# Kernel tuning notes

Measured on AMD Instinct MI355X. Metric: run time of the kernel, lower is better.

The kernel has to match this reference:

```python
import jax, jax.numpy as jnp
import numpy as np

D = 4       # number of TT dimensions
N = 128     # mode size per dimension (Ns)
R = 16      # TT rank (RMAX)
B = 262144  # batch of query points


def setup_inputs() -> dict:
    key = jax.random.key(0)
    ks = jax.random.split(key, 5)
    # points in [-1, 1] (remap_needed=True assumes this domain)
    x = jax.random.uniform(ks[0], (B, D), dtype=jnp.float32) * 2.0 - 1.0
    core0 = jax.random.normal(ks[1], (1, N, R), dtype=jnp.float32)
    core1 = jax.random.normal(ks[2], (R, N, R), dtype=jnp.float32)
    core2 = jax.random.normal(ks[3], (R, N, R), dtype=jnp.float32)
    core3 = jax.random.normal(ks[4], (R, N, 1), dtype=jnp.float32)
    return {"x": x, "core0": core0, "core1": core1, "core2": core2, "core3": core3}


def _forward(x, cores):
    # remap: (x + 1) / 2 * (Ns[0] - 1)  (module uses Ns[0] for all dims)
    n0 = cores[0].shape[1]
    xr = (x + 1.0) * 0.5 * (n0 - 1)
    # per-dim clamp to [0, Ns[i]-1]
    ns = jnp.array([c.shape[1] for c in cores], dtype=x.dtype)  # [D]
    xc = jnp.clip(xr, 0.0, ns - 1.0)  # broadcast over D
    idx_low = jnp.floor(xc).astype(jnp.int32)   # [B, D]
    idx_high = jnp.ceil(xc).astype(jnp.int32)   # [B, D]
    wh = xc - idx_low.astype(x.dtype)           # [B, D] interpolation weights
    # gather + linear interpolation per core -> list of [r_prev, B, r_next]
    newcores = []
    for i, c in enumerate(cores):
        lo = jnp.take(c, idx_low[:, i], axis=1)   # [r_prev, B, r_next]
        hi = jnp.take(c, idx_high[:, i], axis=1)  # [r_prev, B, r_next]
        w = wh[:, i][None, :, None]               # [1, B, 1]
        newcores.append((1.0 - w) * lo + w * hi)
    # chained batched contraction, right to left (matches ttcontract)
    res = newcores[-1]
    for i in range(len(newcores) - 2, 0, -1):
        res = jnp.einsum('abc,cbk->abk', newcores[i], res)
    return jnp.einsum('abc,cbk->b', newcores[0], res)  # [B]


def reference(x, core0, core1, core2, core3):
    return _forward(x, [core0, core1, core2, core3])
```

## Files before the change

### kernel.cpp

```cpp
#include <hip/hip_runtime.h>
#include <hip/hip_bf16.h>

typedef unsigned int uint32;

#define NPT 128
#define RNK 16
#define MIDROW 264
#define MIDROW_U32 132
#define EDGEROW 20
#define SMEM_BYTES (2*NPT*MIDROW*2 + 2*NPT*EDGEROW*4)

__device__ __forceinline__ float bl(uint32 u){ return __uint_as_float(u << 16); }
__device__ __forceinline__ float bh(uint32 u){ return __uint_as_float(u & 0xffff0000u); }

__device__ __forceinline__ float dot16(const float* v, uint4 U0, uint4 U1) {
  float s0 = fmaf(v[1],  bh(U0.x), v[0]*bl(U0.x));
  s0 = fmaf(v[2],  bl(U0.y), s0); s0 = fmaf(v[3],  bh(U0.y), s0);
  float s1 = fmaf(v[5],  bh(U0.z), v[4]*bl(U0.z));
  s1 = fmaf(v[6],  bl(U0.w), s1); s1 = fmaf(v[7],  bh(U0.w), s1);
  float s2 = fmaf(v[9],  bh(U1.x), v[8]*bl(U1.x));
  s2 = fmaf(v[10], bl(U1.y), s2); s2 = fmaf(v[11], bh(U1.y), s2);
  float s3 = fmaf(v[13], bh(U1.z), v[12]*bl(U1.z));
  s3 = fmaf(v[14], bl(U1.w), s3); s3 = fmaf(v[15], bh(U1.w), s3);
  return (s0 + s1) + (s2 + s3);
}

__device__ __forceinline__ void tt_mid(const uint32* __restrict__ base, float xc, float v[16]) {
  int n0 = (int)xc;
  float w = xc - (float)n0;
  int n1 = min(n0 + 1, NPT - 1);
  const uint32* r0 = base + n0 * MIDROW_U32;
  const uint32* r1 = base + n1 * MIDROW_U32;
  float nv[16];
#pragma unroll
  for (int j = 0; j < 16; ++j) {
    const uint4* p0 = (const uint4*)(r0 + j * 8);
    const uint4* p1 = (const uint4*)(r1 + j * 8);
    uint4 A0 = p0[0], A1 = p0[1];
    uint4 B0 = p1[0], B1 = p1[1];
    float a = dot16(v, A0, A1);
    float b = dot16(v, B0, B1);
    nv[j] = fmaf(w, b - a, a);
  }
#pragma unroll
  for (int j = 0; j < 16; ++j) v[j] = nv[j];
}

__device__ __forceinline__ float remap_clamp(float x) {
  float xr = (x + 1.0f) * 0.5f * (float)(NPT - 1);
  return fminf(fmaxf(xr, 0.0f), (float)(NPT - 1));
}

__global__ __launch_bounds__(1024) void tt_kernel(
    const float* __restrict__ x,  const float* __restrict__ g0,
    const float* __restrict__ g1, const float* __restrict__ g2,
    const float* __restrict__ g3, float* __restrict__ out, int npts)
{
  extern __shared__ char smem[];
  unsigned short* c1 = (unsigned short*)smem;
  unsigned short* c2 = c1 + NPT * MIDROW;
  float* c0 = (float*)(c2 + NPT * MIDROW);
  float* c3 = c0 + NPT * EDGEROW;

  for (int t = threadIdx.x; t < RNK * NPT * RNK; t += blockDim.x) {
    int i = t >> 11;
    int n = (t >> 4) & (NPT - 1);
    int j = t & (RNK - 1);
    __hip_bfloat16 h1 = __float2bfloat16(g1[t]);
    __hip_bfloat16 h2 = __float2bfloat16(g2[t]);
    c1[n * MIDROW + j * 16 + i] = *(unsigned short*)&h1;
    c2[n * MIDROW + j * 16 + i] = *(unsigned short*)&h2;
  }
  for (int t = threadIdx.x; t < NPT * RNK; t += blockDim.x) {
    int n = t >> 4;
    int i = t & (RNK - 1);
    c0[n * EDGEROW + i] = g0[t];
    c3[n * EDGEROW + i] = g3[i * NPT + n];
  }
  __syncthreads();

  int p = blockIdx.x * blockDim.x + threadIdx.x;
  if (p >= npts) return;
  float4 xv = reinterpret_cast<const float4*>(x)[p];

  float v[16];
  {
    float xc = remap_clamp(xv.x);
    int n0 = (int)xc; float w = xc - (float)n0; int n1 = min(n0 + 1, NPT - 1);
    const float4* L = (const float4*)(c0 + n0 * EDGEROW);
    const float4* H = (const float4*)(c0 + n1 * EDGEROW);
#pragma unroll
    for (int k = 0; k < 4; ++k) {
      float4 l = L[k], h = H[k];
      v[4*k+0] = fmaf(w, h.x - l.x, l.x);
      v[4*k+1] = fmaf(w, h.y - l.y, l.y);
      v[4*k+2] = fmaf(w, h.z - l.z, l.z);
      v[4*k+3] = fmaf(w, h.w - l.w, l.w);
    }
  }
  tt_mid((const uint32*)c1, remap_clamp(xv.y), v);
  tt_mid((const uint32*)c2, remap_clamp(xv.z), v);
  float acc;
  {
    float xc = remap_clamp(xv.w);
    int n0 = (int)xc; float w = xc - (float)n0; int n1 = min(n0 + 1, NPT - 1);
    const float4* L = (const float4*)(c3 + n0 * EDGEROW);
    const float4* H = (const float4*)(c3 + n1 * EDGEROW);
    float a0 = 0.f, a1 = 0.f, a2 = 0.f, a3 = 0.f;
#pragma unroll
    for (int k = 0; k < 4; ++k) {
      float4 l = L[k], h = H[k];
      a0 = fmaf(v[4*k+0], fmaf(w, h.x - l.x, l.x), a0);
      a1 = fmaf(v[4*k+1], fmaf(w, h.y - l.y, l.y), a1);
      a2 = fmaf(v[4*k+2], fmaf(w, h.z - l.z, l.z), a2);
      a3 = fmaf(v[4*k+3], fmaf(w, h.w - l.w, l.w), a3);
    }
    acc = (a0 + a1) + (a2 + a3);
  }
  out[p] = acc;
}

extern "C" void kernel_launch(void* const* d_in, const int* in_sizes, int n_in,
                              void* d_out, int out_size, void* d_ws, size_t ws_size,
                              hipStream_t stream) {
  const float* x  = (const float*)d_in[0];
  const float* g0 = (const float*)d_in[1];
  const float* g1 = (const float*)d_in[2];
  const float* g2 = (const float*)d_in[3];
  const float* g3 = (const float*)d_in[4];
  float* out = (float*)d_out;

  int B = in_sizes[0] / 4;
  hipFuncSetAttribute(reinterpret_cast<const void*>(tt_kernel),
                      hipFuncAttributeMaxDynamicSharedMemorySize, SMEM_BYTES);
  int block = 1024;
  int grid = (B + block - 1) / block;
  tt_kernel<<<grid, block, SMEM_BYTES, stream>>>(x, g0, g1, g2, g3, out, B);
}
```

Measured before the change: 92.56 us.

## Split each point across 8 lanes with LDS vector exchange and bf16 dot2

Each TT point is now handled by 8 cooperating threads instead of one. Each lane computes 2 of the 16 rank outputs per middle core, and the intermediate vector is exchanged through a per-wave LDS scratch area as packed bf16. The middle cores are stored in a new interleaved layout and, when the builtin is available, use the hardware bf16 dot2 instruction. Each block loops over 8 rounds of 128 points, with a shuffle reduction for the final core. This cuts per-thread register and LDS traffic, but quantizes the intermediate vector to bf16 and adds exchange and synchronisation overhead.

```diff
diff --git a/kernel.cpp b/kernel.cpp
--- a/kernel.cpp
+++ b/kernel.cpp
@@ -2,48 +2,48 @@
 #include <hip/hip_bf16.h>
 
 typedef unsigned int uint32;
+typedef unsigned short u16;
 
 #define NPT 128
 #define RNK 16
-#define MIDROW 264
-#define MIDROW_U32 132
+#define ROW_U16 256
 #define EDGEROW 20
-#define SMEM_BYTES (2*NPT*MIDROW*2 + 2*NPT*EDGEROW*4)
+#define NWAVES 16
+#define SMEM_BYTES (2*NPT*ROW_U16*2 + 2*NPT*EDGEROW*4 + NWAVES*64*4)
+
+#if defined(__has_builtin)
+#if __has_builtin(__builtin_amdgcn_fdot2_f32_bf16)
+#define HAVE_BFDOT2 1
+#endif
+#endif
 
 __device__ __forceinline__ float bl(uint32 u){ return __uint_as_float(u << 16); }
 __device__ __forceinline__ float bh(uint32 u){ return __uint_as_float(u & 0xffff0000u); }
 
-__device__ __forceinline__ float dot16(const float* v, uint4 U0, uint4 U1) {
-  float s0 = fmaf(v[1],  bh(U0.x), v[0]*bl(U0.x));
-  s0 = fmaf(v[2],  bl(U0.y), s0); s0 = fmaf(v[3],  bh(U0.y), s0);
-  float s1 = fmaf(v[5],  bh(U0.z), v[4]*bl(U0.z));
-  s1 = fmaf(v[6],  bl(U0.w), s1); s1 = fmaf(v[7],  bh(U0.w), s1);
-  float s2 = fmaf(v[9],  bh(U1.x), v[8]*bl(U1.x));
-  s2 = fmaf(v[10], bl(U1.y), s2); s2 = fmaf(v[11], bh(U1.y), s2);
-  float s3 = fmaf(v[13], bh(U1.z), v[12]*bl(U1.z));
-  s3 = fmaf(v[14], bl(U1.w), s3); s3 = fmaf(v[15], bh(U1.w), s3);
-  return (s0 + s1) + (s2 + s3);
+#ifdef HAVE_BFDOT2
+typedef __bf16 v2bf __attribute__((ext_vector_type(2)));
+__device__ __forceinline__ v2bf bc(uint32 u){ return __builtin_bit_cast(v2bf, u); }
+__device__ __forceinline__ float dot8(const uint32* vp, uint4 U) {
+  float s = 0.f;
+  s = __builtin_amdgcn_fdot2_f32_bf16(bc(vp[0]), bc(U.x), s, false);
+  s = __builtin_amdgcn_fdot2_f32_bf16(bc(vp[1]), bc(U.y), s, false);
+  s = __builtin_amdgcn_fdot2_f32_bf16(bc(vp[2]), bc(U.z), s, false);
+  s = __builtin_amdgcn_fdot2_f32_bf16(bc(vp[3]), bc(U.w), s, false);
+  return s;
 }
+#else
+__device__ __forceinline__ float dot8(const uint32* vp, uint4 U) {
+  float s = fmaf(bh(vp[0]), bh(U.x), bl(vp[0]) * bl(U.x));
+  s = fmaf(bl(vp[1]), bl(U.y), s); s = fmaf(bh(vp[1]), bh(U.y), s);
+  s = fmaf(bl(vp[2]), bl(U.z), s); s = fmaf(bh(vp[2]), bh(U.z), s);
+  s = fmaf(bl(vp[3]), bl(U.w), s); s = fmaf(bh(vp[3]), bh(U.w), s);
+  return s;
+}
+#endif
 
-__device__ __forceinline__ void tt_mid(const uint32* __restrict__ base, float xc, float v[16]) {
-  int n0 = (int)xc;
-  float w = xc - (float)n0;
-  int n1 = min(n0 + 1, NPT - 1);
-  const uint32* r0 = base + n0 * MIDROW_U32;
-  const uint32* r1 = base + n1 * MIDROW_U32;
-  float nv[16];
-#pragma unroll
-  for (int j = 0; j < 16; ++j) {
-    const uint4* p0 = (const uint4*)(r0 + j * 8);
-    const uint4* p1 = (const uint4*)(r1 + j * 8);
-    uint4 A0 = p0[0], A1 = p0[1];
-    uint4 B0 = p1[0], B1 = p1[1];
-    float a = dot16(v, A0, A1);
-    float b = dot16(v, B0, B1);
-    nv[j] = fmaf(w, b - a, a);
-  }
-#pragma unroll
-  for (int j = 0; j < 16; ++j) v[j] = nv[j];
+__device__ __forceinline__ uint32 packbf(float a, float b) {
+  __hip_bfloat16 l = __float2bfloat16(a), h = __float2bfloat16(b);
+  return (uint32)(*(u16*)&l) | ((uint32)(*(u16*)&h) << 16);
 }
 
 __device__ __forceinline__ float remap_clamp(float x) {
@@ -51,25 +51,63 @@
   return fminf(fmaxf(xr, 0.0f), (float)(NPT - 1));
 }
 
-__global__ __launch_bounds__(1024) void tt_kernel(
+__device__ __forceinline__ void mid_dim(const u16* __restrict__ c, float xc, int q,
+                                        const uint32* vp, float& nv0, float& nv1)
+{
+  int n0 = (int)xc;
+  float w = xc - (float)n0;
+  int n1 = min(n0 + 1, NPT - 1);
+  const uint32* r0 = (const uint32*)(c + n0 * ROW_U16) + q * 4;
+  const uint32* r1 = (const uint32*)(c + n1 * ROW_U16) + q * 4;
+  uint4 A0 = *(const uint4*)(r0);
+  uint4 B0 = *(const uint4*)(r0 + 32);
+  uint4 C0 = *(const uint4*)(r0 + 64);
+  uint4 D0 = *(const uint4*)(r0 + 96);
+  uint4 A1 = *(const uint4*)(r1);
+  uint4 B1 = *(const uint4*)(r1 + 32);
+  uint4 C1 = *(const uint4*)(r1 + 64);
+  uint4 D1 = *(const uint4*)(r1 + 96);
+  float a0 = dot8(vp, A0) + dot8(vp + 4, B0);
+  float a1 = dot8(vp, A1) + dot8(vp + 4, B1);
+  float b0 = dot8(vp, C0) + dot8(vp + 4, D0);
+  float b1 = dot8(vp, C1) + dot8(vp + 4, D1);
+  nv0 = fmaf(w, a1 - a0, a0);
+  nv1 = fmaf(w, b1 - b0, b0);
+}
+
+__device__ __forceinline__ void exchange(uint32* myxch, int lane,
+                                         float nv0, float nv1, uint32* vp)
+{
+  myxch[lane] = packbf(nv0, nv1);
+  __asm__ volatile("s_waitcnt lgkmcnt(0)" ::: "memory");
+  const uint4* b = (const uint4*)(myxch + (lane & 56));
+  uint4 w0 = b[0], w1 = b[1];
+  vp[0] = w0.x; vp[1] = w0.y; vp[2] = w0.z; vp[3] = w0.w;
+  vp[4] = w1.x; vp[5] = w1.y; vp[6] = w1.z; vp[7] = w1.w;
+}
+
+__global__ __launch_bounds__(1024, 4) void tt_kernel(
     const float* __restrict__ x,  const float* __restrict__ g0,
     const float* __restrict__ g1, const float* __restrict__ g2,
     const float* __restrict__ g3, float* __restrict__ out, int npts)
 {
   extern __shared__ char smem[];
-  unsigned short* c1 = (unsigned short*)smem;
-  unsigned short* c2 = c1 + NPT * MIDROW;
-  float* c0 = (float*)(c2 + NPT * MIDROW);
+  u16* c1 = (u16*)smem;
+  u16* c2 = c1 + NPT * ROW_U16;
+  float* c0 = (float*)(c2 + NPT * ROW_U16);
   float* c3 = c0 + NPT * EDGEROW;
+  uint32* xch = (uint32*)(c3 + NPT * EDGEROW);
 
   for (int t = threadIdx.x; t < RNK * NPT * RNK; t += blockDim.x) {
     int i = t >> 11;
     int n = (t >> 4) & (NPT - 1);
     int j = t & (RNK - 1);
+    int slot = (j >> 1) + ((i >> 3) << 3) + ((j & 1) << 4);
+    int off = n * ROW_U16 + slot * 8 + (i & 7);
     __hip_bfloat16 h1 = __float2bfloat16(g1[t]);
     __hip_bfloat16 h2 = __float2bfloat16(g2[t]);
-    c1[n * MIDROW + j * 16 + i] = *(unsigned short*)&h1;
-    c2[n * MIDROW + j * 16 + i] = *(unsigned short*)&h2;
+    c1[off] = *(u16*)&h1;
+    c2[off] = *(u16*)&h2;
   }
   for (int t = threadIdx.x; t < NPT * RNK; t += blockDim.x) {
     int n = t >> 4;
@@ -79,45 +117,44 @@
   }
   __syncthreads();
 
-  int p = blockIdx.x * blockDim.x + threadIdx.x;
-  if (p >= npts) return;
-  float4 xv = reinterpret_cast<const float4*>(x)[p];
+  const int lane = threadIdx.x & 63;
+  const int q = threadIdx.x & 7;
+  uint32* myxch = xch + (threadIdx.x >> 6) * 64;
+  const int ptb = threadIdx.x >> 3;
 
-  float v[16];
-  {
-    float xc = remap_clamp(xv.x);
-    int n0 = (int)xc; float w = xc - (float)n0; int n1 = min(n0 + 1, NPT - 1);
-    const float4* L = (const float4*)(c0 + n0 * EDGEROW);
-    const float4* H = (const float4*)(c0 + n1 * EDGEROW);
-#pragma unroll
-    for (int k = 0; k < 4; ++k) {
-      float4 l = L[k], h = H[k];
-      v[4*k+0] = fmaf(w, h.x - l.x, l.x);
-      v[4*k+1] = fmaf(w, h.y - l.y, l.y);
-      v[4*k+2] = fmaf(w, h.z - l.z, l.z);
-      v[4*k+3] = fmaf(w, h.w - l.w, l.w);
+  for (int it = 0; it < 8; ++it) {
+    int p = (blockIdx.x << 10) + (it << 7) + ptb;
+    if (p >= npts) break;
+    float4 xv = reinterpret_cast<const float4*>(x)[p];
+
+    uint32 vp[8];
+    float nv0, nv1;
+    {
+      float xc = remap_clamp(xv.x);
+      int n0 = (int)xc; float w = xc - (float)n0; int n1 = min(n0 + 1, NPT - 1);
+      float2 lo = *(const float2*)(c0 + n0 * EDGEROW + 2 * q);
+      float2 hi = *(const float2*)(c0 + n1 * EDGEROW + 2 * q);
+      nv0 = fmaf(w, hi.x - lo.x, lo.x);
+      nv1 = fmaf(w, hi.y - lo.y, lo.y);
+    }
+    exchange(myxch, lane, nv0, nv1, vp);
+    mid_dim(c1, remap_clamp(xv.y), q, vp, nv0, nv1);
+    exchange(myxch, lane, nv0, nv1, vp);
+    mid_dim(c2, remap_clamp(xv.z), q, vp, nv0, nv1);
+    {
+      float xc = remap_clamp(xv.w);
+      int n0 = (int)xc; float w = xc - (float)n0; int n1 = min(n0 + 1, NPT - 1);
+      float2 lo = *(const float2*)(c3 + n0 * EDGEROW + 2 * q);
+      float2 hi = *(const float2*)(c3 + n1 * EDGEROW + 2 * q);
+      float m0 = fmaf(w, hi.x - lo.x, lo.x);
+      float m1 = fmaf(w, hi.y - lo.y, lo.y);
+      float part = fmaf(nv1, m1, nv0 * m0);
+      part += __shfl_xor(part, 1, 64);
+      part += __shfl_xor(part, 2, 64);
+      part += __shfl_xor(part, 4, 64);
+      if (q == 0) out[p] = part;
     }
   }
-  tt_mid((const uint32*)c1, remap_clamp(xv.y), v);
-  tt_mid((const uint32*)c2, remap_clamp(xv.z), v);
-  float acc;
-  {
-    float xc = remap_clamp(xv.w);
-    int n0 = (int)xc; float w = xc - (float)n0; int n1 = min(n0 + 1, NPT - 1);
-    const float4* L = (const float4*)(c3 + n0 * EDGEROW);
-    const float4* H = (const float4*)(c3 + n1 * EDGEROW);
-    float a0 = 0.f, a1 = 0.f, a2 = 0.f, a3 = 0.f;
-#pragma unroll
-    for (int k = 0; k < 4; ++k) {
-      float4 l = L[k], h = H[k];
-      a0 = fmaf(v[4*k+0], fmaf(w, h.x - l.x, l.x), a0);
-      a1 = fmaf(v[4*k+1], fmaf(w, h.y - l.y, l.y), a1);
-      a2 = fmaf(v[4*k+2], fmaf(w, h.z - l.z, l.z), a2);
-      a3 = fmaf(v[4*k+3], fmaf(w, h.w - l.w, l.w), a3);
-    }
-    acc = (a0 + a1) + (a2 + a3);
-  }
-  out[p] = acc;
 }
 
 extern "C" void kernel_launch(void* const* d_in, const int* in_sizes, int n_in,
@@ -134,6 +171,6 @@
   hipFuncSetAttribute(reinterpret_cast<const void*>(tt_kernel),
                       hipFuncAttributeMaxDynamicSharedMemorySize, SMEM_BYTES);
   int block = 1024;
-  int grid = (B + block - 1) / block;
+  int grid = (B + 1024 - 1) / 1024;
   tt_kernel<<<grid, block, SMEM_BYTES, stream>>>(x, g0, g1, g2, g3, out, B);
 }
```

After: 85.47 us. -7.7%, faster.
